# Optimization experiments

Hardware: AMD Instinct MI355X
Metric: run time of the kernel (lower is better)

## Reference

```python
import jax, jax.numpy as jnp
import numpy as np


def setup_inputs() -> dict:
    key = jax.random.key(0)
    kx, ka = jax.random.split(key)
    B, N, F = 8, 2048, 64
    x = jax.random.normal(kx, (B, N, F), dtype=jnp.float32)
    a = jax.random.uniform(ka, (B, N, N), dtype=jnp.float32)  # adjacency weights in [0,1)
    return {"x": x, "a": a}


def reference(x, a):
    # t[b,i,f] = sum_j a[b,i,j] * x[b,j,f]
    t = jnp.einsum("bij,bjf->bif", a, x)
    # MAX/IND: 1.0 where aggregated signal exceeds 0.5, else 0.0
    # (faithful to tf.where(t>0.5, t/t, t*0.0))
    out = jnp.where(t > 0.5, t / t, t * 0.0)
    return out
```

## Files before the change

kernel.cpp:

```cpp
#include <hip/hip_runtime.h>

#define BATCH 8
#define NROW  2048
#define NF    64
#define JSPLIT 4
#define JPB   (NROW / JSPLIT)
#define CHUNK 32
#define TOT   ((size_t)BATCH * NROW * NF)

typedef float  f32x4  __attribute__((ext_vector_type(4)));
typedef __bf16 bf16x8 __attribute__((ext_vector_type(8)));
typedef unsigned short u16x8 __attribute__((ext_vector_type(8)));

union frag_cast { u16x8 u; bf16x8 b; };

#define AS1 __attribute__((address_space(1)))
#define AS3 __attribute__((address_space(3)))

__device__ __forceinline__ void gld16u(const unsigned short* g, unsigned short* l) {
  __builtin_amdgcn_global_load_lds((const AS1 void*)g, (AS3 void*)l, 16, 0, 0);
}
__device__ __forceinline__ float ubits(unsigned u) {
  union { unsigned u; float f; } c; c.u = u; return c.f;
}
__device__ __forceinline__ unsigned fbits(float f) {
  union { float f; unsigned u; } c; c.f = f; return c.u;
}

__global__ __launch_bounds__(256, 4)
void prep_x(const float* __restrict__ xg, unsigned short* __restrict__ xs) {
  __shared__ float t[64][65];
  const int b  = blockIdx.y;
  const int j0 = blockIdx.x * 64;
  const int l  = threadIdx.x & 63;
  const int g  = threadIdx.x >> 6;
  const float* src = xg + ((size_t)b * NROW + j0) * NF;
#pragma unroll
  for (int k = 0; k < 16; ++k) {
    const int j = g * 16 + k;
    t[j][l] = src[(size_t)j * NF + l];
  }
  __syncthreads();
#pragma unroll
  for (int k = 0; k < 16; ++k) {
    const int f = g * 16 + k;
    const float v = t[l][f];
    const unsigned u0 = fbits(v);
    const float f0 = ubits(u0 & 0xFFFF0000u);
    const float r  = v - f0;
    const unsigned u1 = fbits(r);
    const float f1 = ubits(u1 & 0xFFFF0000u);
    const float r2 = r - f1;
    const unsigned u2 = fbits(r2);
    const unsigned short s2 =
        (unsigned short)((u2 + 0x7FFFu + ((u2 >> 16) & 1u)) >> 16);
    const size_t o = ((size_t)b * NF + f) * NROW + j0 + l;
    xs[o]           = (unsigned short)(u0 >> 16);
    xs[o + TOT]     = (unsigned short)(u1 >> 16);
    xs[o + 2 * TOT] = s2;
  }
}

__device__ __forceinline__ void split8(const f32x4 q0, const f32x4 q1,
                                       frag_cast* Af) {
  float av[8];
  *(f32x4*)&av[0] = q0;
  *(f32x4*)&av[4] = q1;
  u16x8 h0, h1, h2;
#pragma unroll
  for (int e = 0; e < 8; ++e) {
    const unsigned u0 = fbits(av[e]);
    const float f0 = ubits(u0 & 0xFFFF0000u);
    const float r  = av[e] - f0;
    const unsigned u1 = fbits(r);
    const float f1 = ubits(u1 & 0xFFFF0000u);
    const float r2 = r - f1;
    const unsigned u2 = fbits(r2);
    h0[e] = (unsigned short)(u0 >> 16);
    h1[e] = (unsigned short)(u1 >> 16);
    h2[e] = (unsigned short)((u2 + 0x7FFFu + ((u2 >> 16) & 1u)) >> 16);
  }
  Af[0].u = h0; Af[1].u = h1; Af[2].u = h2;
}

template <bool DIRECT>
__global__ __launch_bounds__(256, 4)
void gemm_mfma(const float* __restrict__ ag, const unsigned short* __restrict__ xs,
               float* __restrict__ outg, float* __restrict__ wp) {
  __shared__ __align__(16) unsigned short sB[2][3 * 64 * CHUNK];

  const int tid  = threadIdx.x;
  const int ln   = tid & 63;
  const int wv   = tid >> 6;
  const int ln15 = ln & 15;
  const int g    = ln >> 4;
  const int bkey = (ln15 >> 1) & 3;

  const int flat = blockIdx.x;
  const int b    = flat & 7;
  const int rr   = flat >> 3;
  const int bx   = rr & 31;
  const int z    = DIRECT ? 0 : ((rr >> 5) & 3);
  const int i0   = bx * 64;
  const int jb   = z * JPB;
  const int nch  = (DIRECT ? NROW : JPB) / CHUNK;

  const float* aA =
      ag + ((size_t)b * NROW + i0 + wv * 16 + ln15) * NROW + jb + g * 8;
  const unsigned short* xB = xs + (size_t)b * NF * NROW;

  auto stageB = [&](int buf, int j0) {
#pragma unroll
    for (int lvl = 0; lvl < 3; ++lvl) {
      const int n = tid >> 2;
      const int q = (tid & 3) ^ ((n >> 1) & 3);
      gld16u(xB + (size_t)lvl * TOT + (size_t)n * NROW + j0 + q * 8,
             &sB[buf][0] + (lvl * 256 + wv * 64) * 8);
    }
  };

  double macc[4][4];
#pragma unroll
  for (int i = 0; i < 4; ++i)
#pragma unroll
    for (int j = 0; j < 4; ++j) macc[i][j] = 0.0;

  constexpr int AI[6] = {2, 0, 1, 1, 0, 0};
  constexpr int BI[6] = {0, 2, 1, 0, 1, 0};

  stageB(0, jb);
  f32x4 Aa0 = *(const f32x4*)(aA);
  f32x4 Aa1 = *(const f32x4*)(aA + 4);
  f32x4 Ab0 = *(const f32x4*)(aA + CHUNK);
  f32x4 Ab1 = *(const f32x4*)(aA + CHUNK + 4);

  auto body = [&](int t, f32x4& Ar0, f32x4& Ar1) {
    asm volatile("s_waitcnt vmcnt(2)" ::: "memory");
    __builtin_amdgcn_s_barrier();
    __builtin_amdgcn_sched_barrier(0);

    const int tn = (t + 1 < nch) ? (t + 1) : (nch - 1);
    stageB((t + 1) & 1, jb + tn * CHUNK);

    frag_cast Af[3];
    split8(Ar0, Ar1, Af);
    const int tn2 = (t + 2 < nch) ? (t + 2) : (nch - 1);
    Ar0 = *(const f32x4*)(aA + (size_t)tn2 * CHUNK);
    Ar1 = *(const f32x4*)(aA + (size_t)tn2 * CHUNK + 4);

    const unsigned short* sBb = &sB[t & 1][0];
    f32x4 c[4];
#pragma unroll
    for (int nt = 0; nt < 4; ++nt) c[nt] = (f32x4){0.f, 0.f, 0.f, 0.f};

#pragma unroll
    for (int ng = 0; ng < 2; ++ng) {
      frag_cast Bv[2][3];
#pragma unroll
      for (int nn = 0; nn < 2; ++nn) {
        const int ncol = (ng * 2 + nn) * 16 + ln15;
        const int bq   = g ^ bkey;
#pragma unroll
        for (int lvl = 0; lvl < 3; ++lvl)
          Bv[nn][lvl].u = *(const u16x8*)(sBb + lvl * 2048 + ncol * 32 + bq * 8);
      }
#pragma unroll
      for (int term = 0; term < 6; ++term)
#pragma unroll
        for (int nn = 0; nn < 2; ++nn) {
          const int nt = ng * 2 + nn;
          c[nt] = __builtin_amdgcn_mfma_f32_16x16x32_bf16(
              Af[AI[term]].b, Bv[nn][BI[term]].b, c[nt], 0, 0, 0);
        }
    }
#pragma unroll
    for (int nt = 0; nt < 4; ++nt) {
      macc[nt][0] += (double)c[nt].x;
      macc[nt][1] += (double)c[nt].y;
      macc[nt][2] += (double)c[nt].z;
      macc[nt][3] += (double)c[nt].w;
    }
  };

#pragma unroll 1
  for (int t = 0; t < nch; t += 2) {
    body(t, Aa0, Aa1);
    body(t + 1, Ab0, Ab1);
  }

  if (DIRECT) {
#pragma unroll
    for (int nt = 0; nt < 4; ++nt)
#pragma unroll
      for (int r = 0; r < 4; ++r)
        outg[((size_t)b * NROW + i0 + wv * 16 + g * 4 + r) * NF + nt * 16 + ln15] =
            (macc[nt][r] > 0.5) ? 1.0f : 0.0f;
  } else {
    float* wb = wp + (size_t)z * TOT;
#pragma unroll
    for (int nt = 0; nt < 4; ++nt)
#pragma unroll
      for (int r = 0; r < 4; ++r)
        wb[((size_t)b * NROW + i0 + wv * 16 + g * 4 + r) * NF + nt * 16 + ln15] =
            (float)macc[nt][r];
  }
}

__global__ __launch_bounds__(256)
void combine_thresh(const float* __restrict__ wsv, float* __restrict__ outg) {
  const size_t e = ((size_t)blockIdx.x * 256 + threadIdx.x) * 4;
  f32x4 p0 = *(const f32x4*)(wsv + e);
  f32x4 p1 = *(const f32x4*)(wsv + e + TOT);
  f32x4 p2 = *(const f32x4*)(wsv + e + 2 * TOT);
  f32x4 p3 = *(const f32x4*)(wsv + e + 3 * TOT);
  f32x4 o;
  o.x = (((double)p0.x + p1.x + p2.x + p3.x) > 0.5) ? 1.0f : 0.0f;
  o.y = (((double)p0.y + p1.y + p2.y + p3.y) > 0.5) ? 1.0f : 0.0f;
  o.z = (((double)p0.z + p1.z + p2.z + p3.z) > 0.5) ? 1.0f : 0.0f;
  o.w = (((double)p0.w + p1.w + p2.w + p3.w) > 0.5) ? 1.0f : 0.0f;
  *(f32x4*)(outg + e) = o;
}

extern "C" void kernel_launch(void* const* d_in, const int* in_sizes, int n_in,
                              void* d_out, int out_size, void* d_ws, size_t ws_size,
                              hipStream_t stream) {
  const float* x = (const float*)d_in[0];
  const float* a = (const float*)d_in[1];
  float* out = (float*)d_out;
  unsigned short* xs = (unsigned short*)d_ws;
  float* wp = (float*)((char*)d_ws + 3 * TOT * sizeof(unsigned short));

  prep_x<<<dim3(NROW / 64, BATCH), dim3(256), 0, stream>>>(x, xs);

  const size_t need = 3 * TOT * sizeof(unsigned short)
                    + (size_t)JSPLIT * TOT * sizeof(float);
  if (ws_size >= need) {
    gemm_mfma<false><<<dim3(JSPLIT * BATCH * (NROW / 64)), dim3(256), 0, stream>>>(
        a, xs, out, wp);
    combine_thresh<<<dim3((unsigned)(TOT / 1024)), dim3(256), 0, stream>>>(wp, out);
  } else {
    gemm_mfma<true><<<dim3(BATCH * (NROW / 64)), dim3(256), 0, stream>>>(
        a, xs, out, nullptr);
  }
}
```

Measured before the change: 47.68 us.

## Quad-buffer B tiles in LDS and process two chunks per barrier

The LDS staging for the bf16-split X operand goes from double to quad buffering. Each loop iteration prefetches two chunks ahead (B via global_load_lds, A via registers), computes two chunks, then does a single waitcnt and barrier, which halves the number of barriers. The LDS footprint doubles, so the occupancy hint in launch bounds drops from 4 to 3 blocks per CU. Fewer resident waves could reduce latency hiding.

Result: no change. 47.72 us (+0.1%).

```diff
diff --git a/kernel.cpp b/kernel.cpp
--- a/kernel.cpp
+++ b/kernel.cpp
@@ -84,10 +84,10 @@
 }
 
 template <bool DIRECT>
-__global__ __launch_bounds__(256, 4)
+__global__ __launch_bounds__(256, 3)
 void gemm_mfma(const float* __restrict__ ag, const unsigned short* __restrict__ xs,
                float* __restrict__ outg, float* __restrict__ wp) {
-  __shared__ __align__(16) unsigned short sB[2][3 * 64 * CHUNK];
+  __shared__ __align__(16) unsigned short sB[4][3 * 64 * CHUNK];
 
   const int tid  = threadIdx.x;
   const int ln   = tid & 63;
@@ -128,31 +128,13 @@
   constexpr int AI[6] = {2, 0, 1, 1, 0, 0};
   constexpr int BI[6] = {0, 2, 1, 0, 1, 0};
 
-  stageB(0, jb);
-  f32x4 Aa0 = *(const f32x4*)(aA);
-  f32x4 Aa1 = *(const f32x4*)(aA + 4);
-  f32x4 Ab0 = *(const f32x4*)(aA + CHUNK);
-  f32x4 Ab1 = *(const f32x4*)(aA + CHUNK + 4);
-
-  auto body = [&](int t, f32x4& Ar0, f32x4& Ar1) {
-    asm volatile("s_waitcnt vmcnt(2)" ::: "memory");
-    __builtin_amdgcn_s_barrier();
-    __builtin_amdgcn_sched_barrier(0);
-
-    const int tn = (t + 1 < nch) ? (t + 1) : (nch - 1);
-    stageB((t + 1) & 1, jb + tn * CHUNK);
-
+  auto compute = [&](int c, const f32x4 Ar0, const f32x4 Ar1) {
+    const unsigned short* sBb = &sB[c & 3][0];
     frag_cast Af[3];
     split8(Ar0, Ar1, Af);
-    const int tn2 = (t + 2 < nch) ? (t + 2) : (nch - 1);
-    Ar0 = *(const f32x4*)(aA + (size_t)tn2 * CHUNK);
-    Ar1 = *(const f32x4*)(aA + (size_t)tn2 * CHUNK + 4);
-
-    const unsigned short* sBb = &sB[t & 1][0];
-    f32x4 c[4];
-#pragma unroll
-    for (int nt = 0; nt < 4; ++nt) c[nt] = (f32x4){0.f, 0.f, 0.f, 0.f};
-
+    f32x4 cc[4];
+#pragma unroll
+    for (int nt = 0; nt < 4; ++nt) cc[nt] = (f32x4){0.f, 0.f, 0.f, 0.f};
 #pragma unroll
     for (int ng = 0; ng < 2; ++ng) {
       frag_cast Bv[2][3];
@@ -169,23 +151,51 @@
 #pragma unroll
         for (int nn = 0; nn < 2; ++nn) {
           const int nt = ng * 2 + nn;
-          c[nt] = __builtin_amdgcn_mfma_f32_16x16x32_bf16(
-              Af[AI[term]].b, Bv[nn][BI[term]].b, c[nt], 0, 0, 0);
+          cc[nt] = __builtin_amdgcn_mfma_f32_16x16x32_bf16(
+              Af[AI[term]].b, Bv[nn][BI[term]].b, cc[nt], 0, 0, 0);
         }
     }
 #pragma unroll
     for (int nt = 0; nt < 4; ++nt) {
-      macc[nt][0] += (double)c[nt].x;
-      macc[nt][1] += (double)c[nt].y;
-      macc[nt][2] += (double)c[nt].z;
-      macc[nt][3] += (double)c[nt].w;
+      macc[nt][0] += (double)cc[nt].x;
+      macc[nt][1] += (double)cc[nt].y;
+      macc[nt][2] += (double)cc[nt].z;
+      macc[nt][3] += (double)cc[nt].w;
     }
   };
 
+  stageB(0, jb);
+  stageB(1, jb + CHUNK);
+  f32x4 Ae0 = *(const f32x4*)(aA);
+  f32x4 Ae1 = *(const f32x4*)(aA + 4);
+  f32x4 Ao0 = *(const f32x4*)(aA + CHUNK);
+  f32x4 Ao1 = *(const f32x4*)(aA + CHUNK + 4);
+  asm volatile("s_waitcnt vmcnt(4)" ::: "memory");
+  __builtin_amdgcn_s_barrier();
+  __builtin_amdgcn_sched_barrier(0);
+
+  const int nper = nch / 2;
 #pragma unroll 1
-  for (int t = 0; t < nch; t += 2) {
-    body(t, Aa0, Aa1);
-    body(t + 1, Ab0, Ab1);
+  for (int u = 0; u < nper; ++u) {
+    const int c0 = 2 * u, c1 = 2 * u + 1;
+    const int s0 = (c0 + 2 < nch) ? c0 + 2 : nch - 1;
+    const int s1 = (c1 + 2 < nch) ? c1 + 2 : nch - 1;
+
+    stageB((c0 + 2) & 3, jb + s0 * CHUNK);
+    stageB((c1 + 2) & 3, jb + s1 * CHUNK);
+    f32x4 An0 = *(const f32x4*)(aA + (size_t)s0 * CHUNK);
+    f32x4 An1 = *(const f32x4*)(aA + (size_t)s0 * CHUNK + 4);
+    f32x4 Am0 = *(const f32x4*)(aA + (size_t)s1 * CHUNK);
+    f32x4 Am1 = *(const f32x4*)(aA + (size_t)s1 * CHUNK + 4);
+
+    compute(c0, Ae0, Ae1);
+    compute(c1, Ao0, Ao1);
+
+    Ae0 = An0; Ae1 = An1; Ao0 = Am0; Ao1 = Am1;
+
+    asm volatile("s_waitcnt vmcnt(4)" ::: "memory");
+    __builtin_amdgcn_s_barrier();
+    __builtin_amdgcn_sched_barrier(0);
   }
 
   if (DIRECT) {
```

## Halve row tile, split waves across columns, reduce J-split to two

Applied to the files above, without the earlier changes.

Each block now covers 32 rows instead of 64. The four waves are arranged as a 2x2 grid of rows by column halves, so each wave computes two 16-column tiles rather than four. The K split drops from 4 to 2, which halves the partial-sum workspace traffic and the combine reads, while launching twice as many row tiles. The pipeline is simplified to a single-stage A prefetch with __syncthreads in place of the manual vmcnt/double-A scheme. The bf16 split now uses native casts, which round the first two levels instead of truncating them. This lowers per-wave register use but reduces how far A loads are prefetched ahead.

Result: slower. 84.17 us (+76.5%).

```diff
diff --git a/kernel.cpp b/kernel.cpp
--- a/kernel.cpp
+++ b/kernel.cpp
@@ -3,7 +3,7 @@
 #define BATCH 8
 #define NROW  2048
 #define NF    64
-#define JSPLIT 4
+#define JSPLIT 2
 #define JPB   (NROW / JSPLIT)
 #define CHUNK 32
 #define TOT   ((size_t)BATCH * NROW * NF)
@@ -13,18 +13,13 @@
 typedef unsigned short u16x8 __attribute__((ext_vector_type(8)));
 
 union frag_cast { u16x8 u; bf16x8 b; };
+union hbits { __bf16 h; unsigned short u; };
 
 #define AS1 __attribute__((address_space(1)))
 #define AS3 __attribute__((address_space(3)))
 
 __device__ __forceinline__ void gld16u(const unsigned short* g, unsigned short* l) {
   __builtin_amdgcn_global_load_lds((const AS1 void*)g, (AS3 void*)l, 16, 0, 0);
-}
-__device__ __forceinline__ float ubits(unsigned u) {
-  union { unsigned u; float f; } c; c.u = u; return c.f;
-}
-__device__ __forceinline__ unsigned fbits(float f) {
-  union { float f; unsigned u; } c; c.f = f; return c.u;
 }
 
 __global__ __launch_bounds__(256, 4)
@@ -45,19 +40,16 @@
   for (int k = 0; k < 16; ++k) {
     const int f = g * 16 + k;
     const float v = t[l][f];
-    const unsigned u0 = fbits(v);
-    const float f0 = ubits(u0 & 0xFFFF0000u);
-    const float r  = v - f0;
-    const unsigned u1 = fbits(r);
-    const float f1 = ubits(u1 & 0xFFFF0000u);
-    const float r2 = r - f1;
-    const unsigned u2 = fbits(r2);
-    const unsigned short s2 =
-        (unsigned short)((u2 + 0x7FFFu + ((u2 >> 16) & 1u)) >> 16);
+    hbits b0, b1, b2;
+    b0.h = (__bf16)v;
+    const float r  = v - (float)b0.h;
+    b1.h = (__bf16)r;
+    const float r2 = r - (float)b1.h;
+    b2.h = (__bf16)r2;
     const size_t o = ((size_t)b * NF + f) * NROW + j0 + l;
-    xs[o]           = (unsigned short)(u0 >> 16);
-    xs[o + TOT]     = (unsigned short)(u1 >> 16);
-    xs[o + 2 * TOT] = s2;
+    xs[o]           = b0.u;
+    xs[o + TOT]     = b1.u;
+    xs[o + 2 * TOT] = b2.u;
   }
 }
 
@@ -66,21 +58,16 @@
   float av[8];
   *(f32x4*)&av[0] = q0;
   *(f32x4*)&av[4] = q1;
-  u16x8 h0, h1, h2;
+  bf16x8 h0, h1, h2;
 #pragma unroll
   for (int e = 0; e < 8; ++e) {
-    const unsigned u0 = fbits(av[e]);
-    const float f0 = ubits(u0 & 0xFFFF0000u);
-    const float r  = av[e] - f0;
-    const unsigned u1 = fbits(r);
-    const float f1 = ubits(u1 & 0xFFFF0000u);
-    const float r2 = r - f1;
-    const unsigned u2 = fbits(r2);
-    h0[e] = (unsigned short)(u0 >> 16);
-    h1[e] = (unsigned short)(u1 >> 16);
-    h2[e] = (unsigned short)((u2 + 0x7FFFu + ((u2 >> 16) & 1u)) >> 16);
-  }
-  Af[0].u = h0; Af[1].u = h1; Af[2].u = h2;
+    const __bf16 b0 = (__bf16)av[e];
+    const float  r  = av[e] - (float)b0;
+    const __bf16 b1 = (__bf16)r;
+    const float  r2 = r - (float)b1;
+    h0[e] = b0; h1[e] = b1; h2[e] = (__bf16)r2;
+  }
+  Af[0].b = h0; Af[1].b = h1; Af[2].b = h2;
 }
 
 template <bool DIRECT>
@@ -94,20 +81,25 @@
   const int wv   = tid >> 6;
   const int ln15 = ln & 15;
   const int g    = ln >> 4;
+  const int rowq = wv & 1;
+  const int colh = wv >> 1;
   const int bkey = (ln15 >> 1) & 3;
 
   const int flat = blockIdx.x;
   const int b    = flat & 7;
   const int rr   = flat >> 3;
-  const int bx   = rr & 31;
-  const int z    = DIRECT ? 0 : ((rr >> 5) & 3);
-  const int i0   = bx * 64;
-  const int jb   = z * JPB;
+  const int bx   = rr & 63;
+  const int z    = DIRECT ? 0 : (rr >> 6);
+  const int i0   = bx * 32;
+  const int jb   = z * (DIRECT ? 0 : JPB);
   const int nch  = (DIRECT ? NROW : JPB) / CHUNK;
 
   const float* aA =
-      ag + ((size_t)b * NROW + i0 + wv * 16 + ln15) * NROW + jb + g * 8;
+      ag + ((size_t)b * NROW + i0 + rowq * 16 + ln15) * NROW + jb + g * 8;
   const unsigned short* xB = xs + (size_t)b * NF * NROW;
+
+  const int boff = (colh * 32 + ln15) * 32 + (g ^ bkey) * 8;
+  const unsigned short* pBr[2] = { &sB[0][boff], &sB[1][boff] };
 
   auto stageB = [&](int buf, int j0) {
 #pragma unroll
@@ -119,9 +111,9 @@
     }
   };
 
-  double macc[4][4];
-#pragma unroll
-  for (int i = 0; i < 4; ++i)
+  double macc[2][4];
+#pragma unroll
+  for (int i = 0; i < 2; ++i)
 #pragma unroll
     for (int j = 0; j < 4; ++j) macc[i][j] = 0.0;
 
@@ -129,80 +121,63 @@
   constexpr int BI[6] = {0, 2, 1, 0, 1, 0};
 
   stageB(0, jb);
-  f32x4 Aa0 = *(const f32x4*)(aA);
-  f32x4 Aa1 = *(const f32x4*)(aA + 4);
-  f32x4 Ab0 = *(const f32x4*)(aA + CHUNK);
-  f32x4 Ab1 = *(const f32x4*)(aA + CHUNK + 4);
-
-  auto body = [&](int t, f32x4& Ar0, f32x4& Ar1) {
-    asm volatile("s_waitcnt vmcnt(2)" ::: "memory");
-    __builtin_amdgcn_s_barrier();
-    __builtin_amdgcn_sched_barrier(0);
-
-    const int tn = (t + 1 < nch) ? (t + 1) : (nch - 1);
-    stageB((t + 1) & 1, jb + tn * CHUNK);
+  f32x4 A0 = *(const f32x4*)(aA);
+  f32x4 A1 = *(const f32x4*)(aA + 4);
+
+#pragma unroll 1
+  for (int t = 0; t < nch; ++t) {
+    __syncthreads();
+    if (t + 1 < nch) stageB((t + 1) & 1, jb + (t + 1) * CHUNK);
+    const int tn = (t + 1 < nch) ? (t + 1) : t;
+    f32x4 N0 = *(const f32x4*)(aA + (size_t)tn * CHUNK);
+    f32x4 N1 = *(const f32x4*)(aA + (size_t)tn * CHUNK + 4);
 
     frag_cast Af[3];
-    split8(Ar0, Ar1, Af);
-    const int tn2 = (t + 2 < nch) ? (t + 2) : (nch - 1);
-    Ar0 = *(const f32x4*)(aA + (size_t)tn2 * CHUNK);
-    Ar1 = *(const f32x4*)(aA + (size_t)tn2 * CHUNK + 4);
-
-    const unsigned short* sBb = &sB[t & 1][0];
-    f32x4 c[4];
-#pragma unroll
-    for (int nt = 0; nt < 4; ++nt) c[nt] = (f32x4){0.f, 0.f, 0.f, 0.f};
-
-#pragma unroll
-    for (int ng = 0; ng < 2; ++ng) {
-      frag_cast Bv[2][3];
-#pragma unroll
-      for (int nn = 0; nn < 2; ++nn) {
-        const int ncol = (ng * 2 + nn) * 16 + ln15;
-        const int bq   = g ^ bkey;
-#pragma unroll
-        for (int lvl = 0; lvl < 3; ++lvl)
-          Bv[nn][lvl].u = *(const u16x8*)(sBb + lvl * 2048 + ncol * 32 + bq * 8);
-      }
-#pragma unroll
-      for (int term = 0; term < 6; ++term)
-#pragma unroll
-        for (int nn = 0; nn < 2; ++nn) {
-          const int nt = ng * 2 + nn;
-          c[nt] = __builtin_amdgcn_mfma_f32_16x16x32_bf16(
-              Af[AI[term]].b, Bv[nn][BI[term]].b, c[nt], 0, 0, 0);
-        }
-    }
-#pragma unroll
-    for (int nt = 0; nt < 4; ++nt) {
+    split8(A0, A1, Af);
+    A0 = N0; A1 = N1;
+
+    const unsigned short* pB = pBr[t & 1];
+    frag_cast Bv[2][3];
+#pragma unroll
+    for (int nt = 0; nt < 2; ++nt)
+#pragma unroll
+      for (int lvl = 0; lvl < 3; ++lvl)
+        Bv[nt][lvl].u = *(const u16x8*)(pB + nt * 512 + lvl * 2048);
+
+    f32x4 c[2];
+    c[0] = (f32x4){0.f, 0.f, 0.f, 0.f};
+    c[1] = (f32x4){0.f, 0.f, 0.f, 0.f};
+#pragma unroll
+    for (int term = 0; term < 6; ++term)
+#pragma unroll
+      for (int nt = 0; nt < 2; ++nt)
+        c[nt] = __builtin_amdgcn_mfma_f32_16x16x32_bf16(
+            Af[AI[term]].b, Bv[nt][BI[term]].b, c[nt], 0, 0, 0);
+
+#pragma unroll
+    for (int nt = 0; nt < 2; ++nt) {
       macc[nt][0] += (double)c[nt].x;
       macc[nt][1] += (double)c[nt].y;
       macc[nt][2] += (double)c[nt].z;
       macc[nt][3] += (double)c[nt].w;
     }
-  };
-
-#pragma unroll 1
-  for (int t = 0; t < nch; t += 2) {
-    body(t, Aa0, Aa1);
-    body(t + 1, Ab0, Ab1);
   }
 
   if (DIRECT) {
 #pragma unroll
-    for (int nt = 0; nt < 4; ++nt)
+    for (int nt = 0; nt < 2; ++nt)
 #pragma unroll
       for (int r = 0; r < 4; ++r)
-        outg[((size_t)b * NROW + i0 + wv * 16 + g * 4 + r) * NF + nt * 16 + ln15] =
-            (macc[nt][r] > 0.5) ? 1.0f : 0.0f;
+        outg[((size_t)b * NROW + i0 + rowq * 16 + g * 4 + r) * NF +
+             colh * 32 + nt * 16 + ln15] = (macc[nt][r] > 0.5) ? 1.0f : 0.0f;
   } else {
     float* wb = wp + (size_t)z * TOT;
 #pragma unroll
-    for (int nt = 0; nt < 4; ++nt)
+    for (int nt = 0; nt < 2; ++nt)
 #pragma unroll
       for (int r = 0; r < 4; ++r)
-        wb[((size_t)b * NROW + i0 + wv * 16 + g * 4 + r) * NF + nt * 16 + ln15] =
-            (float)macc[nt][r];
+        wb[((size_t)b * NROW + i0 + rowq * 16 + g * 4 + r) * NF +
+           colh * 32 + nt * 16 + ln15] = (float)macc[nt][r];
   }
 }
 
@@ -211,13 +186,11 @@
   const size_t e = ((size_t)blockIdx.x * 256 + threadIdx.x) * 4;
   f32x4 p0 = *(const f32x4*)(wsv + e);
   f32x4 p1 = *(const f32x4*)(wsv + e + TOT);
-  f32x4 p2 = *(const f32x4*)(wsv + e + 2 * TOT);
-  f32x4 p3 = *(const f32x4*)(wsv + e + 3 * TOT);
   f32x4 o;
-  o.x = (((double)p0.x + p1.x + p2.x + p3.x) > 0.5) ? 1.0f : 0.0f;
-  o.y = (((double)p0.y + p1.y + p2.y + p3.y) > 0.5) ? 1.0f : 0.0f;
-  o.z = (((double)p0.z + p1.z + p2.z + p3.z) > 0.5) ? 1.0f : 0.0f;
-  o.w = (((double)p0.w + p1.w + p2.w + p3.w) > 0.5) ? 1.0f : 0.0f;
+  o.x = (((double)p0.x + p1.x) > 0.5) ? 1.0f : 0.0f;
+  o.y = (((double)p0.y + p1.y) > 0.5) ? 1.0f : 0.0f;
+  o.z = (((double)p0.z + p1.z) > 0.5) ? 1.0f : 0.0f;
+  o.w = (((double)p0.w + p1.w) > 0.5) ? 1.0f : 0.0f;
   *(f32x4*)(outg + e) = o;
 }
 
@@ -235,11 +208,11 @@
   const size_t need = 3 * TOT * sizeof(unsigned short)
                     + (size_t)JSPLIT * TOT * sizeof(float);
   if (ws_size >= need) {
-    gemm_mfma<false><<<dim3(JSPLIT * BATCH * (NROW / 64)), dim3(256), 0, stream>>>(
+    gemm_mfma<false><<<dim3(JSPLIT * BATCH * (NROW / 32)), dim3(256), 0, stream>>>(
         a, xs, out, wp);
     combine_thresh<<<dim3((unsigned)(TOT / 1024)), dim3(256), 0, stream>>>(wp, out);
   } else {
-    gemm_mfma<true><<<dim3(BATCH * (NROW / 64)), dim3(256), 0, stream>>>(
+    gemm_mfma<true><<<dim3(BATCH * (NROW / 32)), dim3(256), 0, stream>>>(
         a, xs, out, nullptr);
   }
 }
```

## Replace 3-way bf16 split with scaled 2-way fp16 split for MFMA GEMM

Applied to the files above, without the earlier changes.

Switches the error-compensated emulation of fp32 matmul from a three-level bf16 split (six MFMA terms) to a two-level fp16 split with power-of-two scaling (four MFMA terms), scaling the threshold to match. This cuts MFMA work, LDS staging, and workspace for x by a third. It also simplifies the main loop from a manually double-unrolled body with explicit waitcnt to a single-step loop with __syncthreads, which may reduce latency hiding. The fp16 split has fewer mantissa bits and relies on the value range of the inputs to avoid overflow and underflow, so values near the threshold may be classified differently.

Result: faster. 41.28 us (-13.4%).

```diff
diff --git a/kernel.cpp b/kernel.cpp
--- a/kernel.cpp
+++ b/kernel.cpp
@@ -8,23 +8,22 @@
 #define CHUNK 32
 #define TOT   ((size_t)BATCH * NROW * NF)
 
-typedef float  f32x4  __attribute__((ext_vector_type(4)));
-typedef __bf16 bf16x8 __attribute__((ext_vector_type(8)));
+typedef float    f32x4 __attribute__((ext_vector_type(4)));
+typedef _Float16 f16x8 __attribute__((ext_vector_type(8)));
 typedef unsigned short u16x8 __attribute__((ext_vector_type(8)));
 
-union frag_cast { u16x8 u; bf16x8 b; };
+union fragh { u16x8 u; f16x8 h; };
+union hbits { _Float16 h; unsigned short u; };
+
+#define ASCALE 4096.0f
+#define XSCALE 2048.0f
+#define THRESH 4194304.0
 
 #define AS1 __attribute__((address_space(1)))
 #define AS3 __attribute__((address_space(3)))
 
 __device__ __forceinline__ void gld16u(const unsigned short* g, unsigned short* l) {
   __builtin_amdgcn_global_load_lds((const AS1 void*)g, (AS3 void*)l, 16, 0, 0);
-}
-__device__ __forceinline__ float ubits(unsigned u) {
-  union { unsigned u; float f; } c; c.u = u; return c.f;
-}
-__device__ __forceinline__ unsigned fbits(float f) {
-  union { float f; unsigned u; } c; c.f = f; return c.u;
 }
 
 __global__ __launch_bounds__(256, 4)
@@ -44,50 +43,39 @@
 #pragma unroll
   for (int k = 0; k < 16; ++k) {
     const int f = g * 16 + k;
-    const float v = t[l][f];
-    const unsigned u0 = fbits(v);
-    const float f0 = ubits(u0 & 0xFFFF0000u);
-    const float r  = v - f0;
-    const unsigned u1 = fbits(r);
-    const float f1 = ubits(u1 & 0xFFFF0000u);
-    const float r2 = r - f1;
-    const unsigned u2 = fbits(r2);
-    const unsigned short s2 =
-        (unsigned short)((u2 + 0x7FFFu + ((u2 >> 16) & 1u)) >> 16);
+    const float v = t[l][f] * XSCALE;
+    hbits b0, b1;
+    b0.h = (_Float16)v;
+    const float r = v - (float)b0.h;
+    b1.h = (_Float16)r;
     const size_t o = ((size_t)b * NF + f) * NROW + j0 + l;
-    xs[o]           = (unsigned short)(u0 >> 16);
-    xs[o + TOT]     = (unsigned short)(u1 >> 16);
-    xs[o + 2 * TOT] = s2;
-  }
-}
-
-__device__ __forceinline__ void split8(const f32x4 q0, const f32x4 q1,
-                                       frag_cast* Af) {
+    xs[o]       = b0.u;
+    xs[o + TOT] = b1.u;
+  }
+}
+
+__device__ __forceinline__ void split8h(const f32x4 q0, const f32x4 q1,
+                                        fragh* Af) {
   float av[8];
   *(f32x4*)&av[0] = q0;
   *(f32x4*)&av[4] = q1;
-  u16x8 h0, h1, h2;
+  f16x8 h0, h1;
 #pragma unroll
   for (int e = 0; e < 8; ++e) {
-    const unsigned u0 = fbits(av[e]);
-    const float f0 = ubits(u0 & 0xFFFF0000u);
-    const float r  = av[e] - f0;
-    const unsigned u1 = fbits(r);
-    const float f1 = ubits(u1 & 0xFFFF0000u);
-    const float r2 = r - f1;
-    const unsigned u2 = fbits(r2);
-    h0[e] = (unsigned short)(u0 >> 16);
-    h1[e] = (unsigned short)(u1 >> 16);
-    h2[e] = (unsigned short)((u2 + 0x7FFFu + ((u2 >> 16) & 1u)) >> 16);
-  }
-  Af[0].u = h0; Af[1].u = h1; Af[2].u = h2;
+    const float v = av[e] * ASCALE;
+    const _Float16 b0 = (_Float16)v;
+    const float r = v - (float)b0;
+    h0[e] = b0;
+    h1[e] = (_Float16)r;
+  }
+  Af[0].h = h0; Af[1].h = h1;
 }
 
 template <bool DIRECT>
 __global__ __launch_bounds__(256, 4)
 void gemm_mfma(const float* __restrict__ ag, const unsigned short* __restrict__ xs,
                float* __restrict__ outg, float* __restrict__ wp) {
-  __shared__ __align__(16) unsigned short sB[2][3 * 64 * CHUNK];
+  __shared__ __align__(16) unsigned short sB[2][2 * 64 * CHUNK];
 
   const int tid  = threadIdx.x;
   const int ln   = tid & 63;
@@ -111,7 +99,7 @@
 
   auto stageB = [&](int buf, int j0) {
 #pragma unroll
-    for (int lvl = 0; lvl < 3; ++lvl) {
+    for (int lvl = 0; lvl < 2; ++lvl) {
       const int n = tid >> 2;
       const int q = (tid & 3) ^ ((n >> 1) & 3);
       gld16u(xB + (size_t)lvl * TOT + (size_t)n * NROW + j0 + q * 8,
@@ -125,28 +113,24 @@
 #pragma unroll
     for (int j = 0; j < 4; ++j) macc[i][j] = 0.0;
 
-  constexpr int AI[6] = {2, 0, 1, 1, 0, 0};
-  constexpr int BI[6] = {0, 2, 1, 0, 1, 0};
+  constexpr int AI[4] = {1, 1, 0, 0};
+  constexpr int BI[4] = {1, 0, 1, 0};
 
   stageB(0, jb);
-  f32x4 Aa0 = *(const f32x4*)(aA);
-  f32x4 Aa1 = *(const f32x4*)(aA + 4);
-  f32x4 Ab0 = *(const f32x4*)(aA + CHUNK);
-  f32x4 Ab1 = *(const f32x4*)(aA + CHUNK + 4);
-
-  auto body = [&](int t, f32x4& Ar0, f32x4& Ar1) {
-    asm volatile("s_waitcnt vmcnt(2)" ::: "memory");
-    __builtin_amdgcn_s_barrier();
-    __builtin_amdgcn_sched_barrier(0);
-
-    const int tn = (t + 1 < nch) ? (t + 1) : (nch - 1);
-    stageB((t + 1) & 1, jb + tn * CHUNK);
-
-    frag_cast Af[3];
-    split8(Ar0, Ar1, Af);
-    const int tn2 = (t + 2 < nch) ? (t + 2) : (nch - 1);
-    Ar0 = *(const f32x4*)(aA + (size_t)tn2 * CHUNK);
-    Ar1 = *(const f32x4*)(aA + (size_t)tn2 * CHUNK + 4);
+  f32x4 A0 = *(const f32x4*)(aA);
+  f32x4 A1 = *(const f32x4*)(aA + 4);
+
+#pragma unroll 1
+  for (int t = 0; t < nch; ++t) {
+    __syncthreads();
+    if (t + 1 < nch) stageB((t + 1) & 1, jb + (t + 1) * CHUNK);
+    const int tn = (t + 1 < nch) ? (t + 1) : t;
+    f32x4 N0 = *(const f32x4*)(aA + (size_t)tn * CHUNK);
+    f32x4 N1 = *(const f32x4*)(aA + (size_t)tn * CHUNK + 4);
+
+    fragh Af[2];
+    split8h(A0, A1, Af);
+    A0 = N0; A1 = N1;
 
     const unsigned short* sBb = &sB[t & 1][0];
     f32x4 c[4];
@@ -155,22 +139,22 @@
 
 #pragma unroll
     for (int ng = 0; ng < 2; ++ng) {
-      frag_cast Bv[2][3];
+      fragh Bv[2][2];
 #pragma unroll
       for (int nn = 0; nn < 2; ++nn) {
         const int ncol = (ng * 2 + nn) * 16 + ln15;
         const int bq   = g ^ bkey;
 #pragma unroll
-        for (int lvl = 0; lvl < 3; ++lvl)
+        for (int lvl = 0; lvl < 2; ++lvl)
           Bv[nn][lvl].u = *(const u16x8*)(sBb + lvl * 2048 + ncol * 32 + bq * 8);
       }
 #pragma unroll
-      for (int term = 0; term < 6; ++term)
+      for (int term = 0; term < 4; ++term)
 #pragma unroll
         for (int nn = 0; nn < 2; ++nn) {
           const int nt = ng * 2 + nn;
-          c[nt] = __builtin_amdgcn_mfma_f32_16x16x32_bf16(
-              Af[AI[term]].b, Bv[nn][BI[term]].b, c[nt], 0, 0, 0);
+          c[nt] = __builtin_amdgcn_mfma_f32_16x16x32_f16(
+              Af[AI[term]].h, Bv[nn][BI[term]].h, c[nt], 0, 0, 0);
         }
     }
 #pragma unroll
@@ -180,12 +164,6 @@
       macc[nt][2] += (double)c[nt].z;
       macc[nt][3] += (double)c[nt].w;
     }
-  };
-
-#pragma unroll 1
-  for (int t = 0; t < nch; t += 2) {
-    body(t, Aa0, Aa1);
-    body(t + 1, Ab0, Ab1);
   }
 
   if (DIRECT) {
@@ -194,7 +172,7 @@
 #pragma unroll
       for (int r = 0; r < 4; ++r)
         outg[((size_t)b * NROW + i0 + wv * 16 + g * 4 + r) * NF + nt * 16 + ln15] =
-            (macc[nt][r] > 0.5) ? 1.0f : 0.0f;
+            (macc[nt][r] > THRESH) ? 1.0f : 0.0f;
   } else {
     float* wb = wp + (size_t)z * TOT;
 #pragma unroll
@@ -214,10 +192,10 @@
   f32x4 p2 = *(const f32x4*)(wsv + e + 2 * TOT);
   f32x4 p3 = *(const f32x4*)(wsv + e + 3 * TOT);
   f32x4 o;
-  o.x = (((double)p0.x + p1.x + p2.x + p3.x) > 0.5) ? 1.0f : 0.0f;
-  o.y = (((double)p0.y + p1.y + p2.y + p3.y) > 0.5) ? 1.0f : 0.0f;
-  o.z = (((double)p0.z + p1.z + p2.z + p3.z) > 0.5) ? 1.0f : 0.0f;
-  o.w = (((double)p0.w + p1.w + p2.w + p3.w) > 0.5) ? 1.0f : 0.0f;
+  o.x = (((double)p0.x + p1.x + p2.x + p3.x) > THRESH) ? 1.0f : 0.0f;
+  o.y = (((double)p0.y + p1.y + p2.y + p3.y) > THRESH) ? 1.0f : 0.0f;
+  o.z = (((double)p0.z + p1.z + p2.z + p3.z) > THRESH) ? 1.0f : 0.0f;
+  o.w = (((double)p0.w + p1.w + p2.w + p3.w) > THRESH) ? 1.0f : 0.0f;
   *(f32x4*)(outg + e) = o;
 }
 
@@ -228,11 +206,11 @@
   const float* a = (const float*)d_in[1];
   float* out = (float*)d_out;
   unsigned short* xs = (unsigned short*)d_ws;
-  float* wp = (float*)((char*)d_ws + 3 * TOT * sizeof(unsigned short));
+  float* wp = (float*)((char*)d_ws + 2 * TOT * sizeof(unsigned short));
 
   prep_x<<<dim3(NROW / 64, BATCH), dim3(256), 0, stream>>>(x, xs);
 
-  const size_t need = 3 * TOT * sizeof(unsigned short)
+  const size_t need = 2 * TOT * sizeof(unsigned short)
                     + (size_t)JSPLIT * TOT * sizeof(float);
   if (ws_size >= need) {
     gemm_mfma<false><<<dim3(JSPLIT * BATCH * (NROW / 64)), dim3(256), 0, stream>>>(
```
